# Optimization experiments

Measured on AMD Instinct MI355X. Metric: run time of the kernel, lower is better.

The kernel has to match this reference:

```python
import jax, jax.numpy as jnp
import numpy as np

B, S, D = 8, 4096, 256
NUM_WINDOW = 8
WIN = S // NUM_WINDOW          # 512
H = 2                          # num_heads
K = D                          # key_dim = d_model per source
DFF = 1024
LN_EPS = 1e-3                  # keras LayerNormalization default epsilon


def _layer_norm(x, g, b):
    mu = jnp.mean(x, axis=-1, keepdims=True)
    var = jnp.mean(jnp.square(x - mu), axis=-1, keepdims=True)
    return (x - mu) * jax.lax.rsqrt(var + LN_EPS) * g + b


def setup_inputs() -> dict:
    key = jax.random.key(0)
    ks = jax.random.split(key, 12)
    s = 0.02
    inp = {
        "x": jax.random.normal(ks[0], (B, S, D), dtype=jnp.float32),
        # MHA projections (keras MultiHeadAttention layout)
        "Wq": jax.random.normal(ks[1], (D, H, K), dtype=jnp.float32) * s,
        "bq": jnp.zeros((H, K), dtype=jnp.float32),
        "Wk": jax.random.normal(ks[2], (D, H, K), dtype=jnp.float32) * s,
        "bk": jnp.zeros((H, K), dtype=jnp.float32),
        "Wv": jax.random.normal(ks[3], (D, H, K), dtype=jnp.float32) * s,
        "bv": jnp.zeros((H, K), dtype=jnp.float32),
        "Wo": jax.random.normal(ks[4], (H, K, D), dtype=jnp.float32) * s,
        "bo": jnp.zeros((D,), dtype=jnp.float32),
        "ln1_g": jnp.ones((D,), dtype=jnp.float32),
        "ln1_b": jnp.zeros((D,), dtype=jnp.float32),
        # FeedForward
        "W1": jax.random.normal(ks[5], (D, DFF), dtype=jnp.float32) * s,
        "b1": jnp.zeros((DFF,), dtype=jnp.float32),
        "W2": jax.random.normal(ks[6], (DFF, D), dtype=jnp.float32) * s,
        "b2": jnp.zeros((D,), dtype=jnp.float32),
        "ln2_g": jnp.ones((D,), dtype=jnp.float32),
        "ln2_b": jnp.zeros((D,), dtype=jnp.float32),
    }
    return inp


def reference(x, Wq, bq, Wk, bk, Wv, bv, Wo, bo, ln1_g, ln1_b,
              W1, b1, W2, b2, ln2_g, ln2_b):
    # --- Localized self-attention: block-diagonal over NUM_WINDOW windows ---
    xw = x.reshape(B, NUM_WINDOW, WIN, D)               # [b, w, s, d]
    q = jnp.einsum('bwsd,dhk->bwshk', xw, Wq) + bq      # [b, w, s, h, k]
    k = jnp.einsum('bwsd,dhk->bwshk', xw, Wk) + bk
    v = jnp.einsum('bwsd,dhk->bwshk', xw, Wv) + bv
    scores = jnp.einsum('bwshk,bwthk->bwhst', q, k) / jnp.sqrt(
        jnp.asarray(K, dtype=x.dtype))                  # [b, w, h, s, t]
    attn = jax.nn.softmax(scores, axis=-1)
    ctx = jnp.einsum('bwhst,bwthk->bwshk', attn, v)     # [b, w, s, h, k]
    attn_out = jnp.einsum('bwshk,hkd->bwsd', ctx, Wo) + bo
    attn_out = attn_out.reshape(B, S, D)                # concat over windows
    x = _layer_norm(x + attn_out, ln1_g, ln1_b)
    # --- FeedForward (dropout inactive at inference) ---
    h = jax.nn.relu(x @ W1 + b1)
    ff = h @ W2 + b2
    return _layer_norm(x + ff, ln2_g, ln2_b)
```

## Files before the change

### kernel.cpp

```cpp
#include <hip/hip_runtime.h>

typedef unsigned short u16;
typedef short short8 __attribute__((ext_vector_type(8)));
typedef float f32x4 __attribute__((ext_vector_type(4)));

#define AS1C const __attribute__((address_space(1))) void*
#define AS3P __attribute__((address_space(3))) void*

__device__ __forceinline__ u16 f2b(float f) {
  unsigned u = __float_as_uint(f);
  return (u16)((u + 0x7fffu + ((u >> 16) & 1u)) >> 16);
}
__device__ __forceinline__ float b2f(u16 h) {
  return __uint_as_float((unsigned)h << 16);
}

#define BB 8
#define SS 4096
#define DD 256
#define MTOK (BB*SS)

#define OFF_WQKVT  ((size_t)0)
#define OFF_WOT    ((size_t)786432)
#define OFF_W1T    ((size_t)1048576)
#define OFF_W2T    ((size_t)1572864)
#define OFF_BQKV   ((size_t)2097152)
#define OFF_XB     ((size_t)2103296)
#define OFF_QKV    ((size_t)18880512)
#define OFF_YB     ((size_t)52434944)
#define OFF_HB     ((size_t)69212160)
#define OFF_VT     ((size_t)119543808)
#define OFF_CTX    ((size_t)153098240)

__global__ __launch_bounds__(256) void cast_x_kernel(const float* __restrict__ x,
                                                     u16* __restrict__ xb) {
  size_t i = ((size_t)blockIdx.x * 256 + threadIdx.x) * 4;
  float4 v = *(const float4*)(x + i);
  ushort4 o;
  o.x = f2b(v.x); o.y = f2b(v.y); o.z = f2b(v.z); o.w = f2b(v.w);
  *(ushort4*)(xb + i) = o;
}

__global__ __launch_bounds__(256) void prep_w_kernel(
    const float* __restrict__ Wq, const float* __restrict__ Wk, const float* __restrict__ Wv,
    const float* __restrict__ Wo, const float* __restrict__ W1, const float* __restrict__ W2,
    const float* __restrict__ bq, const float* __restrict__ bk, const float* __restrict__ bv,
    u16* __restrict__ wqkvt, u16* __restrict__ wot, u16* __restrict__ w1t,
    u16* __restrict__ w2t, float* __restrict__ bqkv)
{
  for (int i = blockIdx.x * 256 + threadIdx.x; i < 1050112; i += 1024 * 256) {
    if (i < 393216) {
      int n = i >> 8, d = i & 255;
      const float* W = (n < 512) ? Wq : (n < 1024) ? Wk : Wv;
      int nn = n & 511;
      wqkvt[i] = f2b(W[d * 512 + nn]);
    } else if (i < 524288) {
      int j = i - 393216;
      int dout = j >> 9, hk = j & 511;
      wot[j] = f2b(Wo[hk * 256 + dout]);
    } else if (i < 786432) {
      int j = i - 524288;
      int f = j >> 8, d = j & 255;
      w1t[j] = f2b(W1[d * 1024 + f]);
    } else if (i < 1048576) {
      int j = i - 786432;
      int d = j >> 10, f = j & 1023;
      w2t[j] = f2b(W2[f * 256 + d]);
    } else {
      int n = i - 1048576;
      bqkv[n] = (n < 512) ? bq[n] : (n < 1024) ? bk[n - 512] : bv[n - 1024];
    }
  }
}

__global__ __launch_bounds__(256) void gemm_nres(
    const u16* __restrict__ A, const u16* __restrict__ BT,
    const float* __restrict__ bias, u16* __restrict__ C,
    u16* __restrict__ vt, int N, int vbase, int relu)
{
  __shared__ __align__(16) u16 lds[16384];
  const int tid = threadIdx.x, lane = tid & 63, wid = tid >> 6;
  const int ln = lane & 15, quad = lane >> 4;
  const int pn = blockIdx.x >> 5;
  const int mg = blockIdx.x & 31;
  const int wno = (wid >> 1) << 5;
  const int wmo = (wid & 1) << 4;
  const long mbase = (long)mg << 10;
  const int nb = pn << 6;
  const u16* Bp = BT + (size_t)nb * 256;
  const u16* Ap = A + (size_t)mbase * 256;

#pragma unroll
  for (int p = 0; p < 8; p++) {
    const int s = p * 256 + tid;
    const int row = s >> 5, pc = s & 31;
    const int c = pc ^ (row & 31);
    __builtin_amdgcn_global_load_lds(
        (AS1C)(Bp + (size_t)row * 256 + c * 8), (AS3P)(lds + s * 8), 16, 0, 0);
  }
  __syncthreads();
  short8 breg[2][8];
#pragma unroll
  for (int j = 0; j < 2; j++) {
    const int row = wno + j * 16 + ln;
#pragma unroll
    for (int ks = 0; ks < 8; ks++)
      breg[j][ks] = *(const short8*)(lds + row * 256 + (((ks << 2) + quad) ^ (row & 31)) * 8);
  }
  __syncthreads();

#pragma unroll
  for (int p = 0; p < 4; p++) {
    const int s = p * 256 + tid;
    const int row = s >> 5, pc = s & 31;
    const int c = pc ^ (row & 31);
    __builtin_amdgcn_global_load_lds(
        (AS1C)(Ap + (size_t)row * 256 + c * 8), (AS3P)(lds + s * 8), 16, 0, 0);
  }

  for (int it = 0; it < 32; it++) {
    const int cur = it & 1;
    const u16* Ab = lds + cur * 8192;
    __syncthreads();
    if (it + 1 < 32) {
      const u16* An = Ap + (size_t)(it + 1) * 32 * 256;
      u16* Ax = lds + (cur ^ 1) * 8192;
#pragma unroll
      for (int p = 0; p < 4; p++) {
        const int s = p * 256 + tid;
        const int row = s >> 5, pc = s & 31;
        const int c = pc ^ (row & 31);
        __builtin_amdgcn_global_load_lds(
            (AS1C)(An + (size_t)row * 256 + c * 8), (AS3P)(Ax + s * 8), 16, 0, 0);
      }
    }
    f32x4 acc[2];
    acc[0] = (f32x4){0.f, 0.f, 0.f, 0.f};
    acc[1] = (f32x4){0.f, 0.f, 0.f, 0.f};
    const int r0 = wmo + ln;
#pragma unroll
    for (int ks = 0; ks < 8; ks++) {
      const short8 a0 = *(const short8*)(Ab + r0 * 256 + (((ks << 2) + quad) ^ (r0 & 31)) * 8);
      acc[0] = __builtin_amdgcn_mfma_f32_16x16x32_bf16(breg[0][ks], a0, acc[0], 0, 0, 0);
      acc[1] = __builtin_amdgcn_mfma_f32_16x16x32_bf16(breg[1][ks], a0, acc[1], 0, 0, 0);
    }
    const long m = mbase + it * 32 + wmo + ln;
    if (nb < vbase) {
#pragma unroll
      for (int j = 0; j < 2; j++) {
        const int n0 = nb + wno + j * 16 + quad * 4;
        f32x4 v = acc[j];
        const float4 b4 = *(const float4*)(bias + n0);
        v[0] += b4.x; v[1] += b4.y; v[2] += b4.z; v[3] += b4.w;
        if (relu) {
#pragma unroll
          for (int r = 0; r < 4; r++) v[r] = fmaxf(v[r], 0.f);
        }
        ushort4 ob;
        ob.x = f2b(v[0]); ob.y = f2b(v[1]); ob.z = f2b(v[2]); ob.w = f2b(v[3]);
        *(ushort4*)(C + (size_t)m * N + n0) = ob;
      }
    } else {
      const int bw = (int)(m >> 9), t = (int)(m & 511);
#pragma unroll
      for (int j = 0; j < 2; j++) {
        const int n0 = nb + wno + j * 16 + quad * 4;
        const int rel = n0 - vbase;
        const int h = rel >> 8, k0 = rel & 255;
        u16* vp = vt + (size_t)(bw * 2 + h) * 131072 + (size_t)k0 * 512 + t;
        const float4 b4 = *(const float4*)(bias + n0);
        vp[0]    = f2b(acc[j][0] + b4.x);
        vp[512]  = f2b(acc[j][1] + b4.y);
        vp[1024] = f2b(acc[j][2] + b4.z);
        vp[1536] = f2b(acc[j][3] + b4.w);
      }
    }
  }
}

__global__ __launch_bounds__(512, 4) void attn_fused(const u16* __restrict__ qkv,
                                                     const u16* __restrict__ vt,
                                                     u16* __restrict__ ctx)
{
  __shared__ __align__(16) u16 lds[38912];
  const int tid = threadIdx.x, lane = tid & 63, wid = tid >> 6;
  const int ln = lane & 15, quad = lane >> 4;
  const int bat = blockIdx.x & 127, mt = blockIdx.x >> 7;
  const int bw = bat >> 1, h = bat & 1;
  const u16* Qb = qkv + (size_t)bw * 786432 + (size_t)h * 256 + (size_t)(mt * 64) * 1536;
  const u16* Kb = qkv + (size_t)bw * 786432 + 512 + (size_t)h * 256;
  const u16* Vb = vt + (size_t)bat * 131072;
  const int wn = wid * 64;
  const int qsw = (ln >> 1) & 3;
  float* red1 = (float*)(lds + 36864);
  float* red2 = red1 + 512;

  f32x4 acc[4][4];
#pragma unroll
  for (int i = 0; i < 4; i++)
#pragma unroll
    for (int j = 0; j < 4; j++) acc[i][j] = (f32x4){0.f, 0.f, 0.f, 0.f};

  if (tid < 256) {
    const int row = tid >> 2;
    const int c = (tid & 3) ^ ((row >> 1) & 3);
    __builtin_amdgcn_global_load_lds(
        (AS1C)(Qb + (size_t)row * 1536 + c * 8), (AS3P)(lds + tid * 8), 16, 0, 0);
  }
#pragma unroll
  for (int p = 0; p < 4; p++) {
    const int s = p * 512 + tid;
    const int row = s >> 2;
    const int c = (s & 3) ^ ((row >> 1) & 3);
    __builtin_amdgcn_global_load_lds(
        (AS1C)(Kb + (size_t)row * 1536 + c * 8), (AS3P)(lds + 4096 + s * 8), 16, 0, 0);
  }

  for (int ki = 0; ki < 8; ki++) {
    const int cur = ki & 1;
    __syncthreads();
    if (ki < 7) {
      const int kt = (ki + 1) * 32, nxt = cur ^ 1;
      if (tid < 256) {
        const int row = tid >> 2;
        const int c = (tid & 3) ^ ((row >> 1) & 3);
        __builtin_amdgcn_global_load_lds(
            (AS1C)(Qb + (size_t)row * 1536 + kt + c * 8),
            (AS3P)(lds + nxt * 2048 + tid * 8), 16, 0, 0);
      }
#pragma unroll
      for (int p = 0; p < 4; p++) {
        const int s = p * 512 + tid;
        const int row = s >> 2;
        const int c = (s & 3) ^ ((row >> 1) & 3);
        __builtin_amdgcn_global_load_lds(
            (AS1C)(Kb + (size_t)row * 1536 + kt + c * 8),
            (AS3P)(lds + 4096 + nxt * 16384 + s * 8), 16, 0, 0);
      }
    }
    short8 a[4], b[4];
#pragma unroll
    for (int i = 0; i < 4; i++)
      a[i] = *(const short8*)(lds + cur * 2048 + ((i * 16 + ln) * 4 + (quad ^ qsw)) * 8);
#pragma unroll
    for (int j = 0; j < 4; j++)
      b[j] = *(const short8*)(lds + 4096 + cur * 16384 + ((wn + j * 16 + ln) * 4 + (quad ^ qsw)) * 8);
    __builtin_amdgcn_s_setprio(1);
#pragma unroll
    for (int i = 0; i < 4; i++)
#pragma unroll
      for (int j = 0; j < 4; j++)
        acc[i][j] = __builtin_amdgcn_mfma_f32_16x16x32_bf16(b[j], a[i], acc[i][j], 0, 0, 0);
    __builtin_amdgcn_s_setprio(0);
  }

  float rowmax[4], rowsum[4];
#pragma unroll
  for (int i = 0; i < 4; i++) {
    float m = -1e30f;
#pragma unroll
    for (int j = 0; j < 4; j++)
#pragma unroll
      for (int r = 0; r < 4; r++) m = fmaxf(m, acc[i][j][r]);
    m = fmaxf(m, __shfl_xor(m, 16));
    m = fmaxf(m, __shfl_xor(m, 32));
    if (quad == 0) red1[wid * 64 + i * 16 + ln] = m;
  }
  __syncthreads();

#pragma unroll
  for (int p = 0; p < 4; p++) {
    const int s = p * 512 + tid;
    const int row = s >> 3, pc = s & 7;
    const int cc = pc ^ (row & 7);
    __builtin_amdgcn_global_load_lds(
        (AS1C)(Vb + (size_t)row * 512 + cc * 8), (AS3P)(lds + s * 8), 16, 0, 0);
  }

#pragma unroll
  for (int i = 0; i < 4; i++) {
    float m = -1e30f;
#pragma unroll
    for (int w = 0; w < 8; w++) m = fmaxf(m, red1[w * 64 + i * 16 + ln]);
    rowmax[i] = m;
  }
#pragma unroll
  for (int i = 0; i < 4; i++) {
    float s = 0.f;
#pragma unroll
    for (int j = 0; j < 4; j++)
#pragma unroll
      for (int r = 0; r < 4; r++) {
        const float e = __expf((acc[i][j][r] - rowmax[i]) * 0.0625f);
        acc[i][j][r] = e; s += e;
      }
    s += __shfl_xor(s, 16);
    s += __shfl_xor(s, 32);
    if (quad == 0) red2[wid * 64 + i * 16 + ln] = s;
  }
  __syncthreads();
#pragma unroll
  for (int i = 0; i < 4; i++) {
    float s = 0.f;
#pragma unroll
    for (int w = 0; w < 8; w++) s += red2[w * 64 + i * 16 + ln];
    rowsum[i] = 1.f / s;
  }

  ushort4 pb[4][4];
#pragma unroll
  for (int i = 0; i < 4; i++)
#pragma unroll
    for (int j = 0; j < 4; j++) {
      pb[i][j].x = f2b(acc[i][j][0] * rowsum[i]);
      pb[i][j].y = f2b(acc[i][j][1] * rowsum[i]);
      pb[i][j].z = f2b(acc[i][j][2] * rowsum[i]);
      pb[i][j].w = f2b(acc[i][j][3] * rowsum[i]);
    }

  u16* Pb = lds + 32768;
  const int wno = wid * 32;
  f32x4 o[4][2];
#pragma unroll
  for (int i = 0; i < 4; i++) {
    o[i][0] = (f32x4){0.f, 0.f, 0.f, 0.f};
    o[i][1] = (f32x4){0.f, 0.f, 0.f, 0.f};
  }

  for (int c = 0; c < 8; c++) {
    __syncthreads();
    if (wid == c) {
#pragma unroll
      for (int i = 0; i < 4; i++)
#pragma unroll
        for (int j = 0; j < 4; j++)
          *(ushort4*)(Pb + (i * 16 + ln) * 72 + j * 16 + quad * 4) = pb[i][j];
    }
    __syncthreads();
    if (c < 7) {
      const int nb = (c + 1) & 1;
#pragma unroll
      for (int p = 0; p < 4; p++) {
        const int s = p * 512 + tid;
        const int row = s >> 3, pc = s & 7;
        const int cc = pc ^ (row & 7);
        __builtin_amdgcn_global_load_lds(
            (AS1C)(Vb + (size_t)row * 512 + (c + 1) * 64 + cc * 8),
            (AS3P)(lds + nb * 16384 + s * 8), 16, 0, 0);
      }
    }
    const u16* Vc = lds + (c & 1) * 16384;
    __builtin_amdgcn_s_setprio(1);
#pragma unroll
    for (int ks = 0; ks < 2; ks++) {
      short8 ap[4];
#pragma unroll
      for (int i = 0; i < 4; i++)
        ap[i] = *(const short8*)(Pb + (i * 16 + ln) * 72 + ks * 32 + quad * 8);
#pragma unroll
      for (int j = 0; j < 2; j++) {
        const int kV = wno + j * 16 + ln;
        const short8 bv = *(const short8*)(Vc + kV * 64 + (((ks << 2) + quad) ^ (kV & 7)) * 8);
#pragma unroll
        for (int i = 0; i < 4; i++)
          o[i][j] = __builtin_amdgcn_mfma_f32_16x16x32_bf16(bv, ap[i], o[i][j], 0, 0, 0);
      }
    }
    __builtin_amdgcn_s_setprio(0);
  }

  const size_t tokr0 = (size_t)bw * 512 + mt * 64;
#pragma unroll
  for (int i = 0; i < 4; i++) {
    const size_t row = tokr0 + i * 16 + ln;
#pragma unroll
    for (int j = 0; j < 2; j++) {
      const int col = h * 256 + wno + j * 16 + quad * 4;
      ushort4 ob;
      ob.x = f2b(o[i][j][0]); ob.y = f2b(o[i][j][1]);
      ob.z = f2b(o[i][j][2]); ob.w = f2b(o[i][j][3]);
      *(ushort4*)(ctx + row * 512 + col) = ob;
    }
  }
}

__global__ __launch_bounds__(256) void gemm_ln(
    const u16* __restrict__ A, const u16* __restrict__ BT,
    const float* __restrict__ bias, const u16* __restrict__ residb,
    const float* __restrict__ g, const float* __restrict__ beta,
    float* __restrict__ yout, u16* __restrict__ ybout, int K)
{
  __shared__ __align__(16) u16 As[2][2048];
  __shared__ __align__(16) u16 Bs[2][8192];
  __shared__ float redS[4][64], redQ[4][64];
  const int tid = threadIdx.x, lane = tid & 63, wid = tid >> 6;
  const int ln = lane & 15, quad = lane >> 4;
  const int qsw = (ln >> 1) & 3;
  const long bm = (long)blockIdx.x * 64;
  const int wn = wid * 64;
  const u16* Ab = A + (size_t)bm * K;
  const int nk = K >> 5;

  f32x4 acc[4][4];
#pragma unroll
  for (int i = 0; i < 4; i++)
#pragma unroll
    for (int j = 0; j < 4; j++) acc[i][j] = (f32x4){0.f, 0.f, 0.f, 0.f};

  {
    const int row = tid >> 2;
    const int c = (tid & 3) ^ ((row >> 1) & 3);
    __builtin_amdgcn_global_load_lds(
        (AS1C)(Ab + (size_t)row * K + c * 8), (AS3P)(&As[0][0] + tid * 8), 16, 0, 0);
#pragma unroll
    for (int p = 0; p < 4; p++) {
      const int s = p * 256 + tid;
      const int br = s >> 2;
      const int bc = (s & 3) ^ ((br >> 1) & 3);
      __builtin_amdgcn_global_load_lds(
          (AS1C)(BT + (size_t)br * K + bc * 8), (AS3P)(&Bs[0][0] + s * 8), 16, 0, 0);
    }
  }

  for (int kti = 0; kti < nk; kti++) {
    const int cur = kti & 1;
    __syncthreads();
    if (kti + 1 < nk) {
      const int kt = (kti + 1) * 32, nxt = cur ^ 1;
      const int row = tid >> 2;
      const int c = (tid & 3) ^ ((row >> 1) & 3);
      __builtin_amdgcn_global_load_lds(
          (AS1C)(Ab + (size_t)row * K + kt + c * 8), (AS3P)(&As[nxt][0] + tid * 8), 16, 0, 0);
#pragma unroll
      for (int p = 0; p < 4; p++) {
        const int s = p * 256 + tid;
        const int br = s >> 2;
        const int bc = (s & 3) ^ ((br >> 1) & 3);
        __builtin_amdgcn_global_load_lds(
            (AS1C)(BT + (size_t)br * K + kt + bc * 8), (AS3P)(&Bs[nxt][0] + s * 8), 16, 0, 0);
      }
    }
    short8 a[4], b[4];
#pragma unroll
    for (int i = 0; i < 4; i++)
      a[i] = *(const short8*)(&As[cur][0] + ((i * 16 + ln) * 4 + (quad ^ qsw)) * 8);
#pragma unroll
    for (int j = 0; j < 4; j++)
      b[j] = *(const short8*)(&Bs[cur][0] + ((wn + j * 16 + ln) * 4 + (quad ^ qsw)) * 8);
    __builtin_amdgcn_s_setprio(1);
#pragma unroll
    for (int i = 0; i < 4; i++)
#pragma unroll
      for (int j = 0; j < 4; j++)
        acc[i][j] = __builtin_amdgcn_mfma_f32_16x16x32_bf16(b[j], a[i], acc[i][j], 0, 0, 0);
    __builtin_amdgcn_s_setprio(0);
  }

#pragma unroll
  for (int i = 0; i < 4; i++) {
    const long gm = bm + i * 16 + ln;
    float s = 0.f, q = 0.f;
#pragma unroll
    for (int j = 0; j < 4; j++) {
      const int n0 = wn + j * 16 + quad * 4;
      const float4 b4 = *(const float4*)(bias + n0);
      const ushort4 r4 = *(const ushort4*)(residb + (size_t)gm * 256 + n0);
      acc[i][j][0] += b4.x + b2f(r4.x);
      acc[i][j][1] += b4.y + b2f(r4.y);
      acc[i][j][2] += b4.z + b2f(r4.z);
      acc[i][j][3] += b4.w + b2f(r4.w);
#pragma unroll
      for (int r = 0; r < 4; r++) { s += acc[i][j][r]; q += acc[i][j][r] * acc[i][j][r]; }
    }
    s += __shfl_xor(s, 16); s += __shfl_xor(s, 32);
    q += __shfl_xor(q, 16); q += __shfl_xor(q, 32);
    if (quad == 0) { redS[wid][i * 16 + ln] = s; redQ[wid][i * 16 + ln] = q; }
  }
  __syncthreads();
#pragma unroll
  for (int i = 0; i < 4; i++) {
    const long gm = bm + i * 16 + ln;
    float s = 0.f, q = 0.f;
#pragma unroll
    for (int w = 0; w < 4; w++) { s += redS[w][i * 16 + ln]; q += redQ[w][i * 16 + ln]; }
    const float mu = s * (1.f / 256.f);
    const float inv = rsqrtf(q * (1.f / 256.f) - mu * mu + 1e-3f);
#pragma unroll
    for (int j = 0; j < 4; j++) {
      const int n0 = wn + j * 16 + quad * 4;
      const float4 gg = *(const float4*)(g + n0);
      const float4 bb = *(const float4*)(beta + n0);
      float o0 = (acc[i][j][0] - mu) * inv * gg.x + bb.x;
      float o1 = (acc[i][j][1] - mu) * inv * gg.y + bb.y;
      float o2 = (acc[i][j][2] - mu) * inv * gg.z + bb.z;
      float o3 = (acc[i][j][3] - mu) * inv * gg.w + bb.w;
      const size_t off = (size_t)gm * 256 + n0;
      if (yout) {
        float4 o4; o4.x = o0; o4.y = o1; o4.z = o2; o4.w = o3;
        *(float4*)(yout + off) = o4;
      }
      if (ybout) {
        ushort4 ob;
        ob.x = f2b(o0); ob.y = f2b(o1); ob.z = f2b(o2); ob.w = f2b(o3);
        *(ushort4*)(ybout + off) = ob;
      }
    }
  }
}

extern "C" void kernel_launch(void* const* d_in, const int* in_sizes, int n_in,
                              void* d_out, int out_size, void* d_ws, size_t ws_size,
                              hipStream_t stream) {
  (void)in_sizes; (void)n_in; (void)out_size; (void)ws_size;
  const float* x    = (const float*)d_in[0];
  const float* Wq   = (const float*)d_in[1];
  const float* bq   = (const float*)d_in[2];
  const float* Wk   = (const float*)d_in[3];
  const float* bk   = (const float*)d_in[4];
  const float* Wv   = (const float*)d_in[5];
  const float* bv   = (const float*)d_in[6];
  const float* Wo   = (const float*)d_in[7];
  const float* bo   = (const float*)d_in[8];
  const float* ln1g = (const float*)d_in[9];
  const float* ln1b = (const float*)d_in[10];
  const float* W1   = (const float*)d_in[11];
  const float* b1   = (const float*)d_in[12];
  const float* W2   = (const float*)d_in[13];
  const float* b2   = (const float*)d_in[14];
  const float* ln2g = (const float*)d_in[15];
  const float* ln2b = (const float*)d_in[16];
  float* out = (float*)d_out;

  char* ws = (char*)d_ws;
  u16*   WQKVT = (u16*)(ws + OFF_WQKVT);
  u16*   WOT   = (u16*)(ws + OFF_WOT);
  u16*   W1T   = (u16*)(ws + OFF_W1T);
  u16*   W2T   = (u16*)(ws + OFF_W2T);
  float* BQKV  = (float*)(ws + OFF_BQKV);
  u16*   XB    = (u16*)(ws + OFF_XB);
  u16*   QKV   = (u16*)(ws + OFF_QKV);
  u16*   YB    = (u16*)(ws + OFF_YB);
  u16*   HB    = (u16*)(ws + OFF_HB);
  u16*   VT    = (u16*)(ws + OFF_VT);
  u16*   CTX   = (u16*)(ws + OFF_CTX);

  cast_x_kernel<<<8192, 256, 0, stream>>>(x, XB);
  prep_w_kernel<<<1024, 256, 0, stream>>>(Wq, Wk, Wv, Wo, W1, W2, bq, bk, bv,
                                          WQKVT, WOT, W1T, W2T, BQKV);
  gemm_nres<<<768, 256, 0, stream>>>(XB, WQKVT, BQKV, QKV, VT, 1536, 1024, 0);
  attn_fused<<<1024, 512, 0, stream>>>(QKV, VT, CTX);
  gemm_ln<<<512, 256, 0, stream>>>(CTX, WOT, bo, XB, ln1g, ln1b, nullptr, YB, 512);
  gemm_nres<<<512, 256, 0, stream>>>(YB, W1T, b1, HB, nullptr, 1024, 1 << 30, 1);
  gemm_ln<<<512, 256, 0, stream>>>(HB, W2T, b2, YB, ln2g, ln2b, out, nullptr, 1024);
}
```

Before: 333.4 us.

## Use triple-buffered LDS ring with explicit vmcnt waits in GEMM kernels

Both gemm_nres and gemm_ln move from double buffering with __syncthreads to a three-slot LDS ring that prefetches two k-tiles ahead. Each iteration waits only on a partial vmcnt and then issues a raw s_barrier, so loads stay in flight longer and overlap with the MFMA work. gemm_nres also hoists the bias loads out of the loop. The cost is more LDS, which may lower occupancy, and the hand-counted vmcnt values are fragile: they must match the number of outstanding global and store operations, including the strided V-transpose stores.

```diff
diff --git a/kernel.cpp b/kernel.cpp
--- a/kernel.cpp
+++ b/kernel.cpp
@@ -6,6 +6,8 @@
 
 #define AS1C const __attribute__((address_space(1))) void*
 #define AS3P __attribute__((address_space(3))) void*
+#define VMW(n) asm volatile("s_waitcnt vmcnt(" #n ")" ::: "memory")
+#define SCHEDB() __builtin_amdgcn_sched_barrier(0)
 
 __device__ __forceinline__ u16 f2b(float f) {
   unsigned u = __float_as_uint(f);
@@ -78,7 +80,7 @@
     const float* __restrict__ bias, u16* __restrict__ C,
     u16* __restrict__ vt, int N, int vbase, int relu)
 {
-  __shared__ __align__(16) u16 lds[16384];
+  __shared__ __align__(16) u16 lds[24576];
   const int tid = threadIdx.x, lane = tid & 63, wid = tid >> 6;
   const int ln = lane & 15, quad = lane >> 4;
   const int pn = blockIdx.x >> 5;
@@ -107,24 +109,76 @@
     for (int ks = 0; ks < 8; ks++)
       breg[j][ks] = *(const short8*)(lds + row * 256 + (((ks << 2) + quad) ^ (row & 31)) * 8);
   }
+  const float4 b40 = *(const float4*)(bias + nb + wno + quad * 4);
+  const float4 b41 = *(const float4*)(bias + nb + wno + 16 + quad * 4);
   __syncthreads();
 
 #pragma unroll
-  for (int p = 0; p < 4; p++) {
-    const int s = p * 256 + tid;
-    const int row = s >> 5, pc = s & 31;
-    const int c = pc ^ (row & 31);
-    __builtin_amdgcn_global_load_lds(
-        (AS1C)(Ap + (size_t)row * 256 + c * 8), (AS3P)(lds + s * 8), 16, 0, 0);
+  for (int sl = 0; sl < 2; sl++) {
+    const u16* As = Ap + (size_t)sl * 32 * 256;
+#pragma unroll
+    for (int p = 0; p < 4; p++) {
+      const int s = p * 256 + tid;
+      const int row = s >> 5, pc = s & 31;
+      const int c = pc ^ (row & 31);
+      __builtin_amdgcn_global_load_lds(
+          (AS1C)(As + (size_t)row * 256 + c * 8), (AS3P)(lds + sl * 8192 + s * 8), 16, 0, 0);
+    }
   }
 
   for (int it = 0; it < 32; it++) {
-    const int cur = it & 1;
-    const u16* Ab = lds + cur * 8192;
-    __syncthreads();
-    if (it + 1 < 32) {
-      const u16* An = Ap + (size_t)(it + 1) * 32 * 256;
-      u16* Ax = lds + (cur ^ 1) * 8192;
+    if (it == 0)            VMW(4);
+    else if (it == 31)      VMW(0);
+    else if (nb < vbase)    VMW(6);
+    else                    VMW(12);
+    SCHEDB();
+    __builtin_amdgcn_s_barrier();
+    SCHEDB();
+    const u16* Ab = lds + (it % 3) * 8192;
+    f32x4 acc[2];
+    acc[0] = (f32x4){0.f, 0.f, 0.f, 0.f};
+    acc[1] = (f32x4){0.f, 0.f, 0.f, 0.f};
+    const int r0 = wmo + ln;
+#pragma unroll
+    for (int ks = 0; ks < 8; ks++) {
+      const short8 a0 = *(const short8*)(Ab + r0 * 256 + (((ks << 2) + quad) ^ (r0 & 31)) * 8);
+      acc[0] = __builtin_amdgcn_mfma_f32_16x16x32_bf16(breg[0][ks], a0, acc[0], 0, 0, 0);
+      acc[1] = __builtin_amdgcn_mfma_f32_16x16x32_bf16(breg[1][ks], a0, acc[1], 0, 0, 0);
+    }
+    const long m = mbase + it * 32 + wmo + ln;
+    if (nb < vbase) {
+#pragma unroll
+      for (int j = 0; j < 2; j++) {
+        const int n0 = nb + wno + j * 16 + quad * 4;
+        f32x4 v = acc[j];
+        const float4 b4 = j ? b41 : b40;
+        v[0] += b4.x; v[1] += b4.y; v[2] += b4.z; v[3] += b4.w;
+        if (relu) {
+#pragma unroll
+          for (int r = 0; r < 4; r++) v[r] = fmaxf(v[r], 0.f);
+        }
+        ushort4 ob;
+        ob.x = f2b(v[0]); ob.y = f2b(v[1]); ob.z = f2b(v[2]); ob.w = f2b(v[3]);
+        *(ushort4*)(C + (size_t)m * N + n0) = ob;
+      }
+    } else {
+      const int bw = (int)(m >> 9), t = (int)(m & 511);
+#pragma unroll
+      for (int j = 0; j < 2; j++) {
+        const int n0 = nb + wno + j * 16 + quad * 4;
+        const int rel = n0 - vbase;
+        const int h = rel >> 8, k0 = rel & 255;
+        u16* vp = vt + (size_t)(bw * 2 + h) * 131072 + (size_t)k0 * 512 + t;
+        const float4 b4 = j ? b41 : b40;
+        vp[0]    = f2b(acc[j][0] + b4.x);
+        vp[512]  = f2b(acc[j][1] + b4.y);
+        vp[1024] = f2b(acc[j][2] + b4.z);
+        vp[1536] = f2b(acc[j][3] + b4.w);
+      }
+    }
+    if (it < 30) {
+      const u16* An = Ap + (size_t)(it + 2) * 32 * 256;
+      u16* Ax = lds + ((it + 2) % 3) * 8192;
 #pragma unroll
       for (int p = 0; p < 4; p++) {
         const int s = p * 256 + tid;
@@ -132,47 +186,6 @@
         const int c = pc ^ (row & 31);
         __builtin_amdgcn_global_load_lds(
             (AS1C)(An + (size_t)row * 256 + c * 8), (AS3P)(Ax + s * 8), 16, 0, 0);
-      }
-    }
-    f32x4 acc[2];
-    acc[0] = (f32x4){0.f, 0.f, 0.f, 0.f};
-    acc[1] = (f32x4){0.f, 0.f, 0.f, 0.f};
-    const int r0 = wmo + ln;
-#pragma unroll
-    for (int ks = 0; ks < 8; ks++) {
-      const short8 a0 = *(const short8*)(Ab + r0 * 256 + (((ks << 2) + quad) ^ (r0 & 31)) * 8);
-      acc[0] = __builtin_amdgcn_mfma_f32_16x16x32_bf16(breg[0][ks], a0, acc[0], 0, 0, 0);
-      acc[1] = __builtin_amdgcn_mfma_f32_16x16x32_bf16(breg[1][ks], a0, acc[1], 0, 0, 0);
-    }
-    const long m = mbase + it * 32 + wmo + ln;
-    if (nb < vbase) {
-#pragma unroll
-      for (int j = 0; j < 2; j++) {
-        const int n0 = nb + wno + j * 16 + quad * 4;
-        f32x4 v = acc[j];
-        const float4 b4 = *(const float4*)(bias + n0);
-        v[0] += b4.x; v[1] += b4.y; v[2] += b4.z; v[3] += b4.w;
-        if (relu) {
-#pragma unroll
-          for (int r = 0; r < 4; r++) v[r] = fmaxf(v[r], 0.f);
-        }
-        ushort4 ob;
-        ob.x = f2b(v[0]); ob.y = f2b(v[1]); ob.z = f2b(v[2]); ob.w = f2b(v[3]);
-        *(ushort4*)(C + (size_t)m * N + n0) = ob;
-      }
-    } else {
-      const int bw = (int)(m >> 9), t = (int)(m & 511);
-#pragma unroll
-      for (int j = 0; j < 2; j++) {
-        const int n0 = nb + wno + j * 16 + quad * 4;
-        const int rel = n0 - vbase;
-        const int h = rel >> 8, k0 = rel & 255;
-        u16* vp = vt + (size_t)(bw * 2 + h) * 131072 + (size_t)k0 * 512 + t;
-        const float4 b4 = *(const float4*)(bias + n0);
-        vp[0]    = f2b(acc[j][0] + b4.x);
-        vp[512]  = f2b(acc[j][1] + b4.y);
-        vp[1024] = f2b(acc[j][2] + b4.z);
-        vp[1536] = f2b(acc[j][3] + b4.w);
       }
     }
   }
@@ -390,8 +403,7 @@
     const float* __restrict__ g, const float* __restrict__ beta,
     float* __restrict__ yout, u16* __restrict__ ybout, int K)
 {
-  __shared__ __align__(16) u16 As[2][2048];
-  __shared__ __align__(16) u16 Bs[2][8192];
+  __shared__ __align__(16) u16 ring[3][10240];
   __shared__ float redS[4][64], redQ[4][64];
   const int tid = threadIdx.x, lane = tid & 63, wid = tid >> 6;
   const int ln = lane & 15, quad = lane >> 4;
@@ -407,53 +419,59 @@
 #pragma unroll
     for (int j = 0; j < 4; j++) acc[i][j] = (f32x4){0.f, 0.f, 0.f, 0.f};
 
-  {
+#pragma unroll
+  for (int sl = 0; sl < 2; sl++) {
+    const int kt = sl * 32;
     const int row = tid >> 2;
     const int c = (tid & 3) ^ ((row >> 1) & 3);
     __builtin_amdgcn_global_load_lds(
-        (AS1C)(Ab + (size_t)row * K + c * 8), (AS3P)(&As[0][0] + tid * 8), 16, 0, 0);
+        (AS1C)(Ab + (size_t)row * K + kt + c * 8), (AS3P)(&ring[sl][0] + tid * 8), 16, 0, 0);
 #pragma unroll
     for (int p = 0; p < 4; p++) {
       const int s = p * 256 + tid;
       const int br = s >> 2;
       const int bc = (s & 3) ^ ((br >> 1) & 3);
       __builtin_amdgcn_global_load_lds(
-          (AS1C)(BT + (size_t)br * K + bc * 8), (AS3P)(&Bs[0][0] + s * 8), 16, 0, 0);
+          (AS1C)(BT + (size_t)br * K + kt + bc * 8), (AS3P)(&ring[sl][2048] + s * 8), 16, 0, 0);
     }
   }
 
   for (int kti = 0; kti < nk; kti++) {
-    const int cur = kti & 1;
-    __syncthreads();
-    if (kti + 1 < nk) {
-      const int kt = (kti + 1) * 32, nxt = cur ^ 1;
+    if (kti + 1 < nk) VMW(5); else VMW(0);
+    SCHEDB();
+    __builtin_amdgcn_s_barrier();
+    SCHEDB();
+    const u16* Rc = &ring[kti % 3][0];
+    short8 a[4], b[4];
+#pragma unroll
+    for (int i = 0; i < 4; i++)
+      a[i] = *(const short8*)(Rc + ((i * 16 + ln) * 4 + (quad ^ qsw)) * 8);
+#pragma unroll
+    for (int j = 0; j < 4; j++)
+      b[j] = *(const short8*)(Rc + 2048 + ((wn + j * 16 + ln) * 4 + (quad ^ qsw)) * 8);
+    __builtin_amdgcn_s_setprio(1);
+#pragma unroll
+    for (int i = 0; i < 4; i++)
+#pragma unroll
+      for (int j = 0; j < 4; j++)
+        acc[i][j] = __builtin_amdgcn_mfma_f32_16x16x32_bf16(b[j], a[i], acc[i][j], 0, 0, 0);
+    __builtin_amdgcn_s_setprio(0);
+    if (kti + 2 < nk) {
+      const int kt = (kti + 2) * 32;
+      u16* Rn = &ring[(kti + 2) % 3][0];
       const int row = tid >> 2;
       const int c = (tid & 3) ^ ((row >> 1) & 3);
       __builtin_amdgcn_global_load_lds(
-          (AS1C)(Ab + (size_t)row * K + kt + c * 8), (AS3P)(&As[nxt][0] + tid * 8), 16, 0, 0);
+          (AS1C)(Ab + (size_t)row * K + kt + c * 8), (AS3P)(Rn + tid * 8), 16, 0, 0);
 #pragma unroll
       for (int p = 0; p < 4; p++) {
         const int s = p * 256 + tid;
         const int br = s >> 2;
         const int bc = (s & 3) ^ ((br >> 1) & 3);
         __builtin_amdgcn_global_load_lds(
-            (AS1C)(BT + (size_t)br * K + kt + bc * 8), (AS3P)(&Bs[nxt][0] + s * 8), 16, 0, 0);
-      }
-    }
-    short8 a[4], b[4];
-#pragma unroll
-    for (int i = 0; i < 4; i++)
-      a[i] = *(const short8*)(&As[cur][0] + ((i * 16 + ln) * 4 + (quad ^ qsw)) * 8);
-#pragma unroll
-    for (int j = 0; j < 4; j++)
-      b[j] = *(const short8*)(&Bs[cur][0] + ((wn + j * 16 + ln) * 4 + (quad ^ qsw)) * 8);
-    __builtin_amdgcn_s_setprio(1);
-#pragma unroll
-    for (int i = 0; i < 4; i++)
-#pragma unroll
-      for (int j = 0; j < 4; j++)
-        acc[i][j] = __builtin_amdgcn_mfma_f32_16x16x32_bf16(b[j], a[i], acc[i][j], 0, 0, 0);
-    __builtin_amdgcn_s_setprio(0);
+            (AS1C)(BT + (size_t)br * K + kt + bc * 8), (AS3P)(Rn + 2048 + s * 8), 16, 0, 0);
+      }
+    }
   }
 
 #pragma unroll
```

New measurement: 319.3 us. 4.2% less time.
